# Kernel tuning notes

Measured on AMD Instinct MI355X. Metric: run time of the kernel, lower is better.

Reference implementation:

```python
import jax, jax.numpy as jnp
import numpy as np

D_MODEL = 1024
NUM_HEADS = 16
HEAD_DIM = D_MODEL // NUM_HEADS


def setup_inputs() -> dict:
    key = jax.random.key(0)
    k1, k2, k3, k4, k5 = jax.random.split(key, 5)
    scale = 1.0 / np.sqrt(D_MODEL)
    x = jax.random.normal(k1, (2, 2048, D_MODEL), dtype=jnp.float32)
    Wqkv = jax.random.uniform(k2, (D_MODEL, 3 * D_MODEL), jnp.float32, -scale, scale)
    bqkv = jax.random.uniform(k3, (3 * D_MODEL,), jnp.float32, -scale, scale)
    Wout = jax.random.uniform(k4, (D_MODEL, D_MODEL), jnp.float32, -scale, scale)
    bout = jax.random.uniform(k5, (D_MODEL,), jnp.float32, -scale, scale)
    return {"x": x, "Wqkv": Wqkv, "bqkv": bqkv, "Wout": Wout, "bout": bout}


def reference(x, Wqkv, bqkv, Wout, bout):
    B, S, _ = x.shape
    qkv = x @ Wqkv + bqkv                                   # [B, S, 3*D]
    # reshape to [B, S, H, 3*head_dim] then to [B, H, S, 3*head_dim]
    qkv = qkv.reshape(B, S, NUM_HEADS, 3 * HEAD_DIM).transpose(0, 2, 1, 3)
    q, k, v = jnp.split(qkv, 3, axis=-1)                    # each [B, H, S, hd]
    scaled = jnp.einsum("bhqd,bhkd->bhqk", q, k) / jnp.sqrt(jnp.float32(HEAD_DIM))
    attn = jax.nn.softmax(scaled, axis=-1)                  # [B, H, S, S]
    values = jnp.einsum("bhqk,bhkd->bhqd", attn, v)         # [B, H, S, hd]
    values = values.transpose(0, 2, 1, 3).reshape(B, S, D_MODEL)
    return values @ Wout + bout
```

## Files before the change

### kernel.cpp

```cpp
#include <hip/hip_runtime.h>


typedef __attribute__((ext_vector_type(8)))  short short8;
typedef __attribute__((ext_vector_type(4)))  short short4v;
typedef __attribute__((ext_vector_type(8)))  float float8;
typedef __attribute__((ext_vector_type(4)))  float f32x4;
typedef __attribute__((ext_vector_type(16))) float f32x16;
typedef __attribute__((ext_vector_type(4)))  int   int4v;

#define D_MODEL 1024
#define NHEAD   16
#define HD      64
#define SEQ     2048
#define N3      (3*D_MODEL)
#define MB      (1024*1024)

static __device__ __forceinline__ float bf2f(short s) {
    unsigned u = ((unsigned)(unsigned short)s) << 16;
    return __builtin_bit_cast(float, u);
}
static __device__ __forceinline__ short f2bf(float f) {
    unsigned u = __builtin_bit_cast(unsigned, f);
    u = (u + 0x7fff + ((u >> 16) & 1)) >> 16;
    return (short)u;
}
static __device__ __forceinline__ unsigned pkbf(float a, float b) {
    unsigned ua = __builtin_bit_cast(unsigned, a);
    ua = (ua + 0x7fff + ((ua >> 16) & 1)) >> 16;
    unsigned ub = __builtin_bit_cast(unsigned, b);
    ub = (ub + 0x7fff + ((ub >> 16) & 1)) & 0xffff0000u;
    return ua | ub;
}
static __device__ __forceinline__ void gl16(const short* g, short* l) {
    __builtin_amdgcn_global_load_lds(
        (const __attribute__((address_space(1))) unsigned int*)g,
        (__attribute__((address_space(3))) unsigned int*)l, 16, 0, 0);
}

__global__ __launch_bounds__(256) void prep(
    const float* __restrict__ x, const float* __restrict__ Wqkv,
    const float* __restrict__ Wout,
    short* __restrict__ Xh, short* __restrict__ Xl,
    short* __restrict__ Wh, short* __restrict__ Wl,
    short* __restrict__ Woh, short* __restrict__ Wol)
{
    __shared__ float tile[32][33];
    const int bid = blockIdx.x;
    const int tid = threadIdx.x;

    if (bid < 2048) {
        const int i = (bid * 256 + tid) * 8;
        const float8 v = *(const float8*)&x[i];
        short8 h, l;
#pragma unroll
        for (int j = 0; j < 8; ++j) {
            h[j] = f2bf(v[j]);
            l[j] = f2bf(v[j] - bf2f(h[j]));
        }
        *(short8*)&Xh[i] = h;
        *(short8*)&Xl[i] = l;
        return;
    }

    const float* in; short *hi, *lo; int K, N, bx, by;
    if (bid < 5120) {
        const int b2 = bid - 2048;
        in = Wqkv; hi = Wh; lo = Wl; K = D_MODEL; N = N3;
        bx = b2 % 96; by = b2 / 96;
    } else {
        const int b3 = bid - 5120;
        in = Wout; hi = Woh; lo = Wol; K = D_MODEL; N = D_MODEL;
        bx = b3 & 31; by = b3 >> 5;
    }
    const int n0 = bx * 32, k0 = by * 32;
    const int tx = tid & 31, ty = tid >> 5;
#pragma unroll
    for (int i = 0; i < 4; ++i)
        tile[ty + 8*i][tx] = in[(k0 + ty + 8*i) * N + (n0 + tx)];
    __syncthreads();
#pragma unroll
    for (int i = 0; i < 4; ++i) {
        const float v  = tile[tx][ty + 8*i];
        const short vh = f2bf(v);
        const short vl = f2bf(v - bf2f(vh));
        const int idx  = (n0 + ty + 8*i) * K + (k0 + tx);
        hi[idx] = vh;
        lo[idx] = vl;
    }
}

__global__ __launch_bounds__(256) void qkv_gemm128(
    const short* __restrict__ Xh, const short* __restrict__ Xl,
    const short* __restrict__ Bh, const short* __restrict__ Bl,
    const float* __restrict__ bias,
    short* __restrict__ Qo, short* __restrict__ Ko, short* __restrict__ Vt)
{
    __shared__ short XhS[128*32], XlS[128*32], BhS[128*32], BlS[128*32];

    const int tid  = threadIdx.x;
    const int wave = tid >> 6, lane = tid & 63;
    const int q4 = lane >> 4, l16 = lane & 15;
    const int m0 = blockIdx.y * 128, n0 = blockIdx.x * 128;
    const int rw = (wave & 1) * 64, cw = (wave >> 1) * 64;
    const int trow = tid >> 2;
    const int tcol = (tid & 3) * 8;

    f32x4 acc[4][4];
#pragma unroll
    for (int i = 0; i < 4; ++i)
#pragma unroll
        for (int j = 0; j < 4; ++j) acc[i][j] = (f32x4){0.f, 0.f, 0.f, 0.f};

    for (int kt = 0; kt < D_MODEL; kt += 32) {
        gl16(&Xh[(m0 + trow) * D_MODEL + kt + tcol],      XhS + tid * 8);
        gl16(&Xh[(m0 + 64 + trow) * D_MODEL + kt + tcol], XhS + 2048 + tid * 8);
        gl16(&Xl[(m0 + trow) * D_MODEL + kt + tcol],      XlS + tid * 8);
        gl16(&Xl[(m0 + 64 + trow) * D_MODEL + kt + tcol], XlS + 2048 + tid * 8);
        gl16(&Bh[(n0 + trow) * D_MODEL + kt + tcol],      BhS + tid * 8);
        gl16(&Bh[(n0 + 64 + trow) * D_MODEL + kt + tcol], BhS + 2048 + tid * 8);
        gl16(&Bl[(n0 + trow) * D_MODEL + kt + tcol],      BlS + tid * 8);
        gl16(&Bl[(n0 + 64 + trow) * D_MODEL + kt + tcol], BlS + 2048 + tid * 8);
        __syncthreads();

        short8 ah[4], al[4], bh[4], bl[4];
#pragma unroll
        for (int t = 0; t < 4; ++t) {
            ah[t] = *(const short8*)&XhS[(rw + t * 16 + l16) * 32 + q4 * 8];
            al[t] = *(const short8*)&XlS[(rw + t * 16 + l16) * 32 + q4 * 8];
            bh[t] = *(const short8*)&BhS[(cw + t * 16 + l16) * 32 + q4 * 8];
            bl[t] = *(const short8*)&BlS[(cw + t * 16 + l16) * 32 + q4 * 8];
        }
#pragma unroll
        for (int ti = 0; ti < 4; ++ti)
#pragma unroll
            for (int tj = 0; tj < 4; ++tj) {
                acc[ti][tj] = __builtin_amdgcn_mfma_f32_16x16x32_bf16(ah[ti], bh[tj], acc[ti][tj], 0, 0, 0);
                acc[ti][tj] = __builtin_amdgcn_mfma_f32_16x16x32_bf16(ah[ti], bl[tj], acc[ti][tj], 0, 0, 0);
                acc[ti][tj] = __builtin_amdgcn_mfma_f32_16x16x32_bf16(al[ti], bh[tj], acc[ti][tj], 0, 0, 0);
            }
        __syncthreads();
    }

    const float SCALE_Q = 0.125f * 1.4426950408889634f;
#pragma unroll
    for (int tj = 0; tj < 4; ++tj) {
        const int n = n0 + cw + tj * 16 + l16;
        const int h = n / 192;
        const int jj = n % 192;
        const float bv = bias[n];
#pragma unroll
        for (int ti = 0; ti < 4; ++ti) {
            const int mb = m0 + rw + ti * 16 + q4 * 4;
            const int b = mb >> 11;
            const int s = mb & 2047;
            const int bh_ = b * NHEAD + h;
            if (jj >= 128) {
                short4v v4;
#pragma unroll
                for (int r = 0; r < 4; ++r) v4[r] = f2bf(acc[ti][tj][r] + bv);
                *(short4v*)&Vt[(bh_ * HD + (jj - 128)) * SEQ + s] = v4;
            } else if (jj < 64) {
#pragma unroll
                for (int r = 0; r < 4; ++r)
                    Qo[(bh_ * SEQ + s + r) * HD + jj] = f2bf((acc[ti][tj][r] + bv) * SCALE_Q);
            } else {
#pragma unroll
                for (int r = 0; r < 4; ++r)
                    Ko[(bh_ * SEQ + s + r) * HD + (jj - 64)] = f2bf(acc[ti][tj][r] + bv);
            }
        }
    }
}

__global__ __launch_bounds__(256, 4) void attn_tscore(
    const short* __restrict__ Q, const short* __restrict__ K,
    const short* __restrict__ Vt,
    short* __restrict__ Ch, short* __restrict__ Cl)
{
    __shared__ __attribute__((aligned(16))) char smem[34816];
    short (*Ks)[72] = (short(*)[72])smem;
    short (*Vs)[40] = (short(*)[40])(smem + 4608);

    const int bh = blockIdx.x;
    const int qb = blockIdx.y;
    const int bi = bh >> 4, hi_ = bh & 15;

    const short* Qp  = Q  + bh * SEQ * HD;
    const short* Kp  = K  + bh * SEQ * HD;
    const short* Vtp = Vt + bh * HD * SEQ;

    const int tid  = threadIdx.x;
    const int wave = tid >> 6, lane = tid & 63;
    const int l5 = lane & 31, hf = lane >> 5;
    const int q0w = qb * 128 + wave * 32;

    short8 qf[4];
#pragma unroll
    for (int c = 0; c < 4; ++c)
        qf[c] = *(const short8*)&Qp[(q0w + l5) * HD + c * 16 + hf * 8];

    f32x16 oacc0 = (f32x16)(0.f), oacc1 = (f32x16)(0.f);
    float m = -1.0e30f, l = 0.f;

    const int sKr = tid >> 3, sKc = (tid & 7) * 8;
    const int sVr = tid >> 2, sVc = (tid & 3) * 8;

    for (int kc = 0; kc < 64; ++kc) {
        const int kbase = kc * 32;
        __syncthreads();
        *(short8*)&Ks[sKr][sKc] = *(const short8*)&Kp[(kbase + sKr) * HD + sKc];
        *(short8*)&Vs[sVr][sVc] = *(const short8*)&Vtp[sVr * SEQ + kbase + sVc];
        __syncthreads();

        f32x16 sacc = (f32x16)(0.f);
#pragma unroll
        for (int c = 0; c < 4; ++c) {
            const short8 ka = *(const short8*)&Ks[l5][c * 16 + hf * 8];
            sacc = __builtin_amdgcn_mfma_f32_32x32x16_bf16(ka, qf[c], sacc, 0, 0, 0);
        }

        float a0 = fmaxf(sacc[0], sacc[8]),  a1 = fmaxf(sacc[1], sacc[9]);
        float a2 = fmaxf(sacc[2], sacc[10]), a3 = fmaxf(sacc[3], sacc[11]);
        float a4 = fmaxf(sacc[4], sacc[12]), a5 = fmaxf(sacc[5], sacc[13]);
        float a6 = fmaxf(sacc[6], sacc[14]), a7 = fmaxf(sacc[7], sacc[15]);
        a0 = fmaxf(a0, a4); a1 = fmaxf(a1, a5); a2 = fmaxf(a2, a6); a3 = fmaxf(a3, a7);
        a0 = fmaxf(fmaxf(a0, a1), fmaxf(a2, a3));
        a0 = fmaxf(a0, __shfl_xor(a0, 32, 64));
        const float mnew  = fmaxf(m, a0);
        const float alpha = exp2f(m - mnew);

        float p[16];
#pragma unroll
        for (int i = 0; i < 16; ++i) p[i] = exp2f(sacc[i] - mnew);

        float s0 = p[0]+p[8], s1 = p[1]+p[9], s2 = p[2]+p[10], s3 = p[3]+p[11];
        float s4 = p[4]+p[12], s5 = p[5]+p[13], s6 = p[6]+p[14], s7 = p[7]+p[15];
        s0 += s4; s1 += s5; s2 += s6; s3 += s7;
        float rs = (s0 + s1) + (s2 + s3);
        rs += __shfl_xor(rs, 32, 64);
        l = l * alpha + rs;
        m = mnew;

#pragma unroll
        for (int i = 0; i < 16; ++i) { oacc0[i] *= alpha; oacc1[i] *= alpha; }

        unsigned u0 = pkbf(p[0],  p[1]),  u1 = pkbf(p[2],  p[3]);
        unsigned u2 = pkbf(p[4],  p[5]),  u3 = pkbf(p[6],  p[7]);
        unsigned u4 = pkbf(p[8],  p[9]),  u5 = pkbf(p[10], p[11]);
        unsigned u6 = pkbf(p[12], p[13]), u7 = pkbf(p[14], p[15]);
        const unsigned x0 = __shfl_xor(u0, 32, 64), x1 = __shfl_xor(u1, 32, 64);
        const unsigned x2 = __shfl_xor(u2, 32, 64), x3 = __shfl_xor(u3, 32, 64);
        const unsigned x4 = __shfl_xor(u4, 32, 64), x5 = __shfl_xor(u5, 32, 64);
        const unsigned x6 = __shfl_xor(u6, 32, 64), x7 = __shfl_xor(u7, 32, 64);
        int4v pb0 = (int4v){ (int)(hf ? x2 : u0), (int)(hf ? x3 : u1),
                             (int)(hf ? u2 : x0), (int)(hf ? u3 : x1) };
        int4v pb1 = (int4v){ (int)(hf ? x6 : u4), (int)(hf ? x7 : u5),
                             (int)(hf ? u6 : x4), (int)(hf ? u7 : x5) };
        const short8 pbf0 = __builtin_bit_cast(short8, pb0);
        const short8 pbf1 = __builtin_bit_cast(short8, pb1);

        {
            const short8 va00 = *(const short8*)&Vs[l5][hf * 8];
            const short8 va01 = *(const short8*)&Vs[l5][16 + hf * 8];
            oacc0 = __builtin_amdgcn_mfma_f32_32x32x16_bf16(va00, pbf0, oacc0, 0, 0, 0);
            oacc0 = __builtin_amdgcn_mfma_f32_32x32x16_bf16(va01, pbf1, oacc0, 0, 0, 0);
            const short8 va10 = *(const short8*)&Vs[32 + l5][hf * 8];
            const short8 va11 = *(const short8*)&Vs[32 + l5][16 + hf * 8];
            oacc1 = __builtin_amdgcn_mfma_f32_32x32x16_bf16(va10, pbf0, oacc1, 0, 0, 0);
            oacc1 = __builtin_amdgcn_mfma_f32_32x32x16_bf16(va11, pbf1, oacc1, 0, 0, 0);
        }
    }

    const float inv = 1.0f / l;
#pragma unroll
    for (int i = 0; i < 16; ++i) { oacc0[i] *= inv; oacc1[i] *= inv; }

    __syncthreads();
    float (*epi)[68] = (float(*)[68])(smem + wave * 8704);
#pragma unroll
    for (int r = 0; r < 16; ++r) {
        const int d = (r & 3) + 8 * (r >> 2) + 4 * hf;
        epi[l5][d]      = oacc0[r];
        epi[l5][32 + d] = oacc1[r];
    }
    __builtin_amdgcn_s_waitcnt(0);
#pragma unroll
    for (int pass = 0; pass < 8; ++pass) {
        const int row = pass * 4 + (lane >> 4);
        const int col = (lane & 15) * 4;
        const float4 v = *(const float4*)&epi[row][col];
        const float o[4] = {v.x, v.y, v.z, v.w};
        short4v hh, ll;
#pragma unroll
        for (int i = 0; i < 4; ++i) {
            hh[i] = f2bf(o[i]);
            ll[i] = f2bf(o[i] - bf2f(hh[i]));
        }
        const size_t co = ((size_t)(bi * SEQ + q0w + row)) * D_MODEL + hi_ * HD + col;
        *(short4v*)&Ch[co] = hh;
        *(short4v*)&Cl[co] = ll;
    }
}

__global__ __launch_bounds__(256) void out_gemm128(
    const short* __restrict__ Ah, const short* __restrict__ Al,
    const short* __restrict__ Bh, const short* __restrict__ Bl,
    const float* __restrict__ bias, float* __restrict__ out)
{
    __shared__ short AhS[128*32], AlS[128*32], BhS[128*32], BlS[128*32];

    const int tid  = threadIdx.x;
    const int wave = tid >> 6, lane = tid & 63;
    const int q4 = lane >> 4, l16 = lane & 15;
    const int m0 = blockIdx.y * 128, n0 = blockIdx.x * 128;
    const int rw = (wave & 1) * 64, cw = (wave >> 1) * 64;
    const int trow = tid >> 2;
    const int tcol = (tid & 3) * 8;

    f32x4 acc[4][4];
#pragma unroll
    for (int i = 0; i < 4; ++i)
#pragma unroll
        for (int j = 0; j < 4; ++j) acc[i][j] = (f32x4){0.f, 0.f, 0.f, 0.f};

    for (int kt = 0; kt < D_MODEL; kt += 32) {
        gl16(&Ah[(m0 + trow) * D_MODEL + kt + tcol],      AhS + tid * 8);
        gl16(&Ah[(m0 + 64 + trow) * D_MODEL + kt + tcol], AhS + 2048 + tid * 8);
        gl16(&Al[(m0 + trow) * D_MODEL + kt + tcol],      AlS + tid * 8);
        gl16(&Al[(m0 + 64 + trow) * D_MODEL + kt + tcol], AlS + 2048 + tid * 8);
        gl16(&Bh[(n0 + trow) * D_MODEL + kt + tcol],      BhS + tid * 8);
        gl16(&Bh[(n0 + 64 + trow) * D_MODEL + kt + tcol], BhS + 2048 + tid * 8);
        gl16(&Bl[(n0 + trow) * D_MODEL + kt + tcol],      BlS + tid * 8);
        gl16(&Bl[(n0 + 64 + trow) * D_MODEL + kt + tcol], BlS + 2048 + tid * 8);
        __syncthreads();

        short8 ah[4], al[4], bh[4], bl[4];
#pragma unroll
        for (int t = 0; t < 4; ++t) {
            ah[t] = *(const short8*)&AhS[(rw + t * 16 + l16) * 32 + q4 * 8];
            al[t] = *(const short8*)&AlS[(rw + t * 16 + l16) * 32 + q4 * 8];
            bh[t] = *(const short8*)&BhS[(cw + t * 16 + l16) * 32 + q4 * 8];
            bl[t] = *(const short8*)&BlS[(cw + t * 16 + l16) * 32 + q4 * 8];
        }
#pragma unroll
        for (int ti = 0; ti < 4; ++ti)
#pragma unroll
            for (int tj = 0; tj < 4; ++tj) {
                acc[ti][tj] = __builtin_amdgcn_mfma_f32_16x16x32_bf16(ah[ti], bh[tj], acc[ti][tj], 0, 0, 0);
                acc[ti][tj] = __builtin_amdgcn_mfma_f32_16x16x32_bf16(ah[ti], bl[tj], acc[ti][tj], 0, 0, 0);
                acc[ti][tj] = __builtin_amdgcn_mfma_f32_16x16x32_bf16(al[ti], bh[tj], acc[ti][tj], 0, 0, 0);
            }
        __syncthreads();
    }

#pragma unroll
    for (int tj = 0; tj < 4; ++tj) {
        const int n = n0 + cw + tj * 16 + l16;
        const float bv = bias[n];
#pragma unroll
        for (int ti = 0; ti < 4; ++ti) {
            const int mb = m0 + rw + ti * 16 + q4 * 4;
#pragma unroll
            for (int r = 0; r < 4; ++r)
                out[(mb + r) * D_MODEL + n] = acc[ti][tj][r] + bv;
        }
    }
}

extern "C" void kernel_launch(void* const* d_in, const int* in_sizes, int n_in,
                              void* d_out, int out_size, void* d_ws, size_t ws_size,
                              hipStream_t stream)
{
    const float* x    = (const float*)d_in[0];
    const float* Wqkv = (const float*)d_in[1];
    const float* bqkv = (const float*)d_in[2];
    const float* Wout = (const float*)d_in[3];
    const float* bout = (const float*)d_in[4];
    float* out = (float*)d_out;

    char* ws = (char*)d_ws;
    short* Qb  = (short*)(ws);
    short* Kb  = (short*)(ws +  8*MB);
    short* Vtb = (short*)(ws + 16*MB);
    short* Woh = (short*)(ws + 24*MB);
    short* Wol = (short*)(ws + 26*MB);
    short* Ch  = (short*)(ws + 28*MB);
    short* Cl  = (short*)(ws + 36*MB);
    short* Xh  = (short*)(ws + 44*MB);
    short* Xl  = (short*)(ws + 52*MB);
    short* Wh  = (short*)(ws + 60*MB);
    short* Wl  = (short*)(ws + 66*MB);

    prep<<<6144, 256, 0, stream>>>(x, Wqkv, Wout, Xh, Xl, Wh, Wl, Woh, Wol);
    qkv_gemm128<<<dim3(24, 32), 256, 0, stream>>>(Xh, Xl, Wh, Wl, bqkv, Qb, Kb, Vtb);
    attn_tscore<<<dim3(32, 16), 256, 0, stream>>>(Qb, Kb, Vtb, Ch, Cl);
    out_gemm128<<<dim3(8, 32), 256, 0, stream>>>(Ch, Cl, Woh, Wol, bout, out);
}
```

Measured before the change: 318.3 us.

## Restructure QKV GEMM into 256x192 double-buffered 8-wave tiles with XCD swizzle

Replaces the 128x128 four-wave QKV GEMM with a 512-thread kernel computing 256x192 tiles, so each block covers exactly one head's Q/K/V columns. Shared-memory tiles are double-buffered so global loads for the next k-step overlap the MFMA work on the current one. It also adds priority hints, finer barriers and a block-index swizzle for cache locality. The larger tiles and double buffer use more registers and LDS, which lowers occupancy. The grid shrinks to 256 blocks, which may underfill the CUs.

```diff
diff --git a/kernel.cpp b/kernel.cpp
--- a/kernel.cpp
+++ b/kernel.cpp
@@ -89,71 +89,116 @@
     }
 }
 
-__global__ __launch_bounds__(256) void qkv_gemm128(
+#define QBUF_SH 28672
+#define OFF_AL  8192
+#define OFF_BH  16384
+#define OFF_BL  22528
+
+__global__ __launch_bounds__(512, 2) void qkv_gemm8(
     const short* __restrict__ Xh, const short* __restrict__ Xl,
     const short* __restrict__ Bh, const short* __restrict__ Bl,
     const float* __restrict__ bias,
     short* __restrict__ Qo, short* __restrict__ Ko, short* __restrict__ Vt)
 {
-    __shared__ short XhS[128*32], XlS[128*32], BhS[128*32], BlS[128*32];
+    __shared__ __attribute__((aligned(16))) short smem[2 * QBUF_SH];
 
     const int tid  = threadIdx.x;
     const int wave = tid >> 6, lane = tid & 63;
     const int q4 = lane >> 4, l16 = lane & 15;
-    const int m0 = blockIdx.y * 128, n0 = blockIdx.x * 128;
-    const int rw = (wave & 1) * 64, cw = (wave >> 1) * 64;
-    const int trow = tid >> 2;
-    const int tcol = (tid & 3) * 8;
-
-    f32x4 acc[4][4];
-#pragma unroll
-    for (int i = 0; i < 4; ++i)
-#pragma unroll
-        for (int j = 0; j < 4; ++j) acc[i][j] = (f32x4){0.f, 0.f, 0.f, 0.f};
-
-    for (int kt = 0; kt < D_MODEL; kt += 32) {
-        gl16(&Xh[(m0 + trow) * D_MODEL + kt + tcol],      XhS + tid * 8);
-        gl16(&Xh[(m0 + 64 + trow) * D_MODEL + kt + tcol], XhS + 2048 + tid * 8);
-        gl16(&Xl[(m0 + trow) * D_MODEL + kt + tcol],      XlS + tid * 8);
-        gl16(&Xl[(m0 + 64 + trow) * D_MODEL + kt + tcol], XlS + 2048 + tid * 8);
-        gl16(&Bh[(n0 + trow) * D_MODEL + kt + tcol],      BhS + tid * 8);
-        gl16(&Bh[(n0 + 64 + trow) * D_MODEL + kt + tcol], BhS + 2048 + tid * 8);
-        gl16(&Bl[(n0 + trow) * D_MODEL + kt + tcol],      BlS + tid * 8);
-        gl16(&Bl[(n0 + 64 + trow) * D_MODEL + kt + tcol], BlS + 2048 + tid * 8);
-        __syncthreads();
-
-        short8 ah[4], al[4], bh[4], bl[4];
-#pragma unroll
-        for (int t = 0; t < 4; ++t) {
-            ah[t] = *(const short8*)&XhS[(rw + t * 16 + l16) * 32 + q4 * 8];
-            al[t] = *(const short8*)&XlS[(rw + t * 16 + l16) * 32 + q4 * 8];
-            bh[t] = *(const short8*)&BhS[(cw + t * 16 + l16) * 32 + q4 * 8];
-            bl[t] = *(const short8*)&BlS[(cw + t * 16 + l16) * 32 + q4 * 8];
-        }
-#pragma unroll
-        for (int ti = 0; ti < 4; ++ti)
-#pragma unroll
-            for (int tj = 0; tj < 4; ++tj) {
-                acc[ti][tj] = __builtin_amdgcn_mfma_f32_16x16x32_bf16(ah[ti], bh[tj], acc[ti][tj], 0, 0, 0);
-                acc[ti][tj] = __builtin_amdgcn_mfma_f32_16x16x32_bf16(ah[ti], bl[tj], acc[ti][tj], 0, 0, 0);
-                acc[ti][tj] = __builtin_amdgcn_mfma_f32_16x16x32_bf16(al[ti], bh[tj], acc[ti][tj], 0, 0, 0);
+    const int wr = wave >> 2, wc = wave & 3;
+
+    const int flat = blockIdx.x;
+    const int sw = (flat & 7) * 32 + (flat >> 3);
+    const int mt = sw & 15, nt = sw >> 4;
+    const int m0 = mt * 256, n0 = nt * 192;
+
+    const short* srcp[7];
+#pragma unroll
+    for (int j = 0; j < 7; ++j) {
+        const int id = j * 512 + tid;
+        const short* s;
+        if (id < 1024)      { s = &Xh[(size_t)(m0 + (id >> 2)) * D_MODEL + (id & 3) * 8]; }
+        else if (id < 2048) { const int c = id - 1024; s = &Xl[(size_t)(m0 + (c >> 2)) * D_MODEL + (c & 3) * 8]; }
+        else if (id < 2816) { const int c = id - 2048; s = &Bh[(size_t)(n0 + (c >> 2)) * D_MODEL + (c & 3) * 8]; }
+        else                { const int c = id - 2816; s = &Bl[(size_t)(n0 + (c >> 2)) * D_MODEL + (c & 3) * 8]; }
+        srcp[j] = s;
+    }
+
+    auto stage = [&](int b) {
+#pragma unroll
+        for (int j = 0; j < 7; ++j) {
+            gl16(srcp[j], smem + b * QBUF_SH + (j * 512 + tid) * 8);
+            srcp[j] += 32;
+        }
+    };
+
+    f32x4 acc[8][3];
+#pragma unroll
+    for (int i = 0; i < 8; ++i)
+#pragma unroll
+        for (int j = 0; j < 3; ++j) acc[i][j] = (f32x4){0.f, 0.f, 0.f, 0.f};
+
+    stage(0);
+    asm volatile("s_waitcnt vmcnt(0)" ::: "memory");
+    __builtin_amdgcn_s_barrier();
+
+    for (int t = 0; t < 32; ++t) {
+        const int cur = t & 1;
+        const short* base = smem + cur * QBUF_SH;
+        const short* Ah_s = base;
+        const short* Al_s = base + OFF_AL;
+        const short* Bh_s = base + OFF_BH;
+        const short* Bl_s = base + OFF_BL;
+
+        short8 bhf[3], blf[3];
+#pragma unroll
+        for (int p = 0; p < 4; ++p) {
+            const int r0 = (wr * 128 + (2*p)   * 16 + l16) * 32 + q4 * 8;
+            const int r1 = (wr * 128 + (2*p+1) * 16 + l16) * 32 + q4 * 8;
+            const short8 a0h = *(const short8*)(Ah_s + r0);
+            const short8 a0l = *(const short8*)(Al_s + r0);
+            const short8 a1h = *(const short8*)(Ah_s + r1);
+            const short8 a1l = *(const short8*)(Al_s + r1);
+            if (p == 0) {
+#pragma unroll
+                for (int n = 0; n < 3; ++n) {
+                    const int rb = (wc * 48 + n * 16 + l16) * 32 + q4 * 8;
+                    bhf[n] = *(const short8*)(Bh_s + rb);
+                    blf[n] = *(const short8*)(Bl_s + rb);
+                }
+                if (t < 31) stage(cur ^ 1);
             }
-        __syncthreads();
+            __builtin_amdgcn_s_barrier();
+            asm volatile("s_waitcnt lgkmcnt(0)" ::: "memory");
+            __builtin_amdgcn_sched_barrier(0);
+            __builtin_amdgcn_s_setprio(1);
+#pragma unroll
+            for (int n = 0; n < 3; ++n) {
+                acc[2*p][n]   = __builtin_amdgcn_mfma_f32_16x16x32_bf16(a0h, bhf[n], acc[2*p][n],   0, 0, 0);
+                acc[2*p][n]   = __builtin_amdgcn_mfma_f32_16x16x32_bf16(a0h, blf[n], acc[2*p][n],   0, 0, 0);
+                acc[2*p][n]   = __builtin_amdgcn_mfma_f32_16x16x32_bf16(a0l, bhf[n], acc[2*p][n],   0, 0, 0);
+                acc[2*p+1][n] = __builtin_amdgcn_mfma_f32_16x16x32_bf16(a1h, bhf[n], acc[2*p+1][n], 0, 0, 0);
+                acc[2*p+1][n] = __builtin_amdgcn_mfma_f32_16x16x32_bf16(a1h, blf[n], acc[2*p+1][n], 0, 0, 0);
+                acc[2*p+1][n] = __builtin_amdgcn_mfma_f32_16x16x32_bf16(a1l, bhf[n], acc[2*p+1][n], 0, 0, 0);
+            }
+            __builtin_amdgcn_s_setprio(0);
+            if (p == 3) asm volatile("s_waitcnt vmcnt(0)" ::: "memory");
+            __builtin_amdgcn_s_barrier();
+        }
     }
 
     const float SCALE_Q = 0.125f * 1.4426950408889634f;
 #pragma unroll
-    for (int tj = 0; tj < 4; ++tj) {
-        const int n = n0 + cw + tj * 16 + l16;
-        const int h = n / 192;
-        const int jj = n % 192;
+    for (int tj = 0; tj < 3; ++tj) {
+        const int jj = wc * 48 + tj * 16 + l16;
+        const int n  = nt * 192 + jj;
         const float bv = bias[n];
 #pragma unroll
-        for (int ti = 0; ti < 4; ++ti) {
-            const int mb = m0 + rw + ti * 16 + q4 * 4;
+        for (int ti = 0; ti < 8; ++ti) {
+            const int mb = m0 + wr * 128 + ti * 16 + q4 * 4;
             const int b = mb >> 11;
             const int s = mb & 2047;
-            const int bh_ = b * NHEAD + h;
+            const int bh_ = b * NHEAD + nt;
             if (jj >= 128) {
                 short4v v4;
 #pragma unroll
@@ -392,7 +437,7 @@
     short* Wl  = (short*)(ws + 66*MB);
 
     prep<<<6144, 256, 0, stream>>>(x, Wqkv, Wout, Xh, Xl, Wh, Wl, Woh, Wol);
-    qkv_gemm128<<<dim3(24, 32), 256, 0, stream>>>(Xh, Xl, Wh, Wl, bqkv, Qb, Kb, Vtb);
+    qkv_gemm8<<<dim3(256), 512, 0, stream>>>(Xh, Xl, Wh, Wl, bqkv, Qb, Kb, Vtb);
     attn_tscore<<<dim3(32, 16), 256, 0, stream>>>(Qb, Kb, Vtb, Ch, Cl);
     out_gemm128<<<dim3(8, 32), 256, 0, stream>>>(Ch, Cl, Woh, Wol, bout, out);
 }
```

Measured after the change: 295.7 us. 1.08x faster.
